# Kernel optimization log

Hardware: AMD Instinct MI355X
Metric: run time of the kernel (lower is better)

Reference implementation:

```python
import jax, jax.numpy as jnp
import numpy as np

N_QUBITS = 12
N_LAYERS = 3


def _apply_ry(state, theta, q):
    # state: (2,)*n real statevector; RY on qubit q
    c = jnp.cos(theta * 0.5)
    s = jnp.sin(theta * 0.5)
    st = jnp.moveaxis(state, q, 0)
    st = jnp.stack([c * st[0] - s * st[1], s * st[0] + c * st[1]])
    return jnp.moveaxis(st, 0, q)


def _apply_cz(state, q, r):
    st = jnp.moveaxis(state, (q, r), (0, 1))
    st = st.at[1, 1].multiply(-1.0)
    return jnp.moveaxis(st, (0, 1), (q, r))


def _embed(x, params):
    # angle-embedding ansatz: L layers of RY(theta[l,q]+x[q]) + CZ ring
    n = N_QUBITS
    state = jnp.zeros((2,) * n, dtype=x.dtype).at[(0,) * n].set(1.0)
    for l in range(N_LAYERS):
        for q in range(n):
            state = _apply_ry(state, params[l, q] + x[q], q)
        for q in range(n):
            state = _apply_cz(state, q, (q + 1) % n)
    return state.reshape(-1)  # (2^n,)


def setup_inputs() -> dict:
    key = jax.random.key(0)
    k1, k2, k3 = jax.random.split(key, 3)
    data = jax.random.uniform(k1, (2048, N_QUBITS), dtype=jnp.float32)
    labels = jax.random.randint(k2, (2048,), 0, 2, dtype=jnp.int32)
    params = jax.random.normal(k3, (N_LAYERS, N_QUBITS), dtype=jnp.float32)
    return {"data": data, "labels": labels, "params": params}


def reference(data, labels, params):
    # Psi[i] = U(x_i, params)|0>, k_ij = |<psi_j|psi_i>|^2 (== prob of amp 0 of U^dag(x_j)U(x_i)|0>)
    psi = jax.vmap(_embed, in_axes=(0, None))(data, params)  # (N, 2^n)
    K = jnp.square(psi @ psi.T)                              # (N, N) pairwise kernel
    lab = 2.0 * labels.astype(psi.dtype) - 1.0               # {0,1} -> {-1,+1}
    LL = jnp.outer(lab, lab)
    kernel_polarity = jnp.sum(LL * K)
    square_sum_k = jnp.sum(K * K)
    square_sum_l = jnp.sum(LL * LL)
    return kernel_polarity / jnp.sqrt(square_sum_k * square_sum_l)
```

## Files before the change

kernel.cpp:

```cpp
#include <hip/hip_runtime.h>
#include <math.h>

#define NQ    12
#define DIM   4096
#define K_EXT 4096
#define KSL   1024
#define NSAMP 2048
#define NLAY  3
#define NT2   16
#define NTRI2 136
#define NSLICE 4
#define BK    64

typedef __attribute__((ext_vector_type(8)))  short bf16x8;
typedef __attribute__((ext_vector_type(16))) float floatx16;

__device__ __forceinline__ unsigned short f32_to_bf16(float x) {
    unsigned u = __builtin_bit_cast(unsigned, x);
    u += 0x7FFFu + ((u >> 16) & 1u);
    return (unsigned short)(u >> 16);
}

__device__ __forceinline__ void gl_lds16(const unsigned short* g, unsigned short* l) {
    __builtin_amdgcn_global_load_lds(
        (const __attribute__((address_space(1))) unsigned int*)g,
        (__attribute__((address_space(3))) unsigned int*)l,
        16, 0, 0);
}

__device__ __forceinline__ void tri_decode(int bid, int& bi, int& bj) {
    int i = (int)((33.0 - sqrt(33.0*33.0 - 8.0*(double)bid)) * 0.5);
    int start = i*(33-i)/2;
    while (bid < start)               { --i; start = i*(33-i)/2; }
    while (bid >= start + (NT2 - i))  { start += NT2 - i; ++i; }
    bi = i; bj = i + (bid - start);
}

__global__ __launch_bounds__(256) void sim_kernel(const float* __restrict__ data,
                                                  const float* __restrict__ params,
                                                  unsigned short* __restrict__ pe)
{
    __shared__ float CS[2*36], SN[2*36];
    __shared__ float trans[2][4608];
    const int tid  = threadIdx.x;
    const int wave = tid >> 6, lane = tid & 63;
    const int sidx = wave >> 1;
    const int w    = wave & 1;
    const int smp  = blockIdx.x * 2 + sidx;

    if (w == 0 && lane < NLAY*NQ) {
        const int q = lane % NQ;
        const float th = 0.5f * (params[lane] + data[smp*NQ + q]);
        CS[sidx*36 + lane] = cosf(th);
        SN[sidx*36 + lane] = sinf(th);
    }
    __syncthreads();

    float v[32];

    float* buf = trans[sidx];
    float* wb  = buf + 36*lane + 2304*w;
    const float* rb = buf + ((lane>>2)&15) + 16*w + 36*(lane&3);

    {
        const float* cs = &CS[sidx*36];
        const float* sn = &SN[sidx*36];
        const int hi = (lane >> 2) & 15;
        float fx = ((lane & 1) ? sn[0] : cs[0]) * ((lane & 2) ? sn[1] : cs[1]);
        fx *= ((hi & 1) ? sn[7]  : cs[7]);
        fx *= ((hi & 2) ? sn[8]  : cs[8]);
        fx *= ((hi & 4) ? sn[9]  : cs[9]);
        fx *= ((hi & 8) ? sn[10] : cs[10]);
        fx *= (w ? sn[11] : cs[11]);
        v[0] = fx * cs[2];
        v[1] = fx * sn[2];
        #pragma unroll
        for (int b = 1; b < 5; ++b) {
            const int M = 1 << b;
            #pragma unroll
            for (int r = 0; r < 32; ++r) {
                if (r < M) {
                    v[r | M] = v[r] * sn[2 + b];
                    v[r]     = v[r] * cs[2 + b];
                }
            }
        }
        const int Base = (lane & 3) | (hi << 7) | (w << 11);
        #pragma unroll
        for (int r = 0; r < 32; ++r) {
            const int i  = Base | (r << 2);
            const int t  = ((i >> 1) | (i << 11)) & 0xFFF;
            const int p  = __popc(i & t) & 1;
            v[r] = __builtin_bit_cast(float, __builtin_bit_cast(int, v[r]) ^ (p << 31));
        }
    }

    #pragma unroll 1
    for (int l = 1; l < NLAY; ++l) {
        const float* cs = &CS[sidx*36 + l*NQ];
        const float* sn = &SN[sidx*36 + l*NQ];
        const int even = !(l & 1);

        {
            const int qb = even ? 7 : 2;
            #pragma unroll
            for (int b = 0; b < 5; ++b) {
                const float c = cs[qb + b], s = sn[qb + b];
                const int M = 1 << b;
                #pragma unroll
                for (int r = 0; r < 32; ++r) {
                    if (!(r & M)) {
                        const float a0 = v[r], a1 = v[r | M];
                        v[r]     = c * a0 - s * a1;
                        v[r | M] = s * a0 + c * a1;
                    }
                }
            }
        }
        {
            const float c0 = cs[0], s0 = sn[0];
            const float t0 = (lane & 1) ? s0 : -s0;
            #pragma unroll
            for (int r = 0; r < 32; ++r) {
                const int iv = __builtin_bit_cast(int, v[r]);
                const int pv = __builtin_amdgcn_update_dpp(0, iv, 0xB1, 0xF, 0xF, true);
                v[r] = c0 * v[r] + t0 * __builtin_bit_cast(float, pv);
            }
            const float c1 = cs[1], s1 = sn[1];
            const float t1 = (lane & 2) ? s1 : -s1;
            #pragma unroll
            for (int r = 0; r < 32; ++r) {
                const int iv = __builtin_bit_cast(int, v[r]);
                const int pv = __builtin_amdgcn_update_dpp(0, iv, 0x4E, 0xF, 0xF, true);
                v[r] = c1 * v[r] + t1 * __builtin_bit_cast(float, pv);
            }
        }
        __syncthreads();
        #pragma unroll
        for (int t = 0; t < 8; ++t) {
            float4 q4;
            q4.x = v[4*t]; q4.y = v[4*t+1]; q4.z = v[4*t+2]; q4.w = v[4*t+3];
            *(float4*)&wb[4*t] = q4;
        }
        __syncthreads();
        #pragma unroll
        for (int r = 0; r < 32; ++r)
            v[r] = rb[144*(r & 15) + 2304*(r >> 4)];

        {
            const int qb = even ? 2 : 7;
            #pragma unroll
            for (int b = 0; b < 5; ++b) {
                const float c = cs[qb + b], s = sn[qb + b];
                const int M = 1 << b;
                #pragma unroll
                for (int r = 0; r < 32; ++r) {
                    if (!(r & M)) {
                        const float a0 = v[r], a1 = v[r | M];
                        v[r]     = c * a0 - s * a1;
                        v[r | M] = s * a0 + c * a1;
                    }
                }
            }
        }
        {
            const int Base = even ? ((lane & 3) | (((lane >> 2) & 15) << 7) | (w << 11))
                                  : (lane | (w << 6));
            const int shift = even ? 2 : 7;
            #pragma unroll
            for (int r = 0; r < 32; ++r) {
                const int i  = Base | (r << shift);
                const int t  = ((i >> 1) | (i << 11)) & 0xFFF;
                const int p  = __popc(i & t) & 1;
                v[r] = __builtin_bit_cast(float, __builtin_bit_cast(int, v[r]) ^ (p << 31));
            }
        }
    }

    const int sw = smp & 7;
    const int ell = w*64 + lane;
    unsigned short* outb = pe + (size_t)smp * K_EXT;
    #pragma unroll
    for (int c = 0; c < 4; ++c) {
        uint4 H;
        H.x = (unsigned)f32_to_bf16(v[c*8+0]) | ((unsigned)f32_to_bf16(v[c*8+1]) << 16);
        H.y = (unsigned)f32_to_bf16(v[c*8+2]) | ((unsigned)f32_to_bf16(v[c*8+3]) << 16);
        H.z = (unsigned)f32_to_bf16(v[c*8+4]) | ((unsigned)f32_to_bf16(v[c*8+5]) << 16);
        H.w = (unsigned)f32_to_bf16(v[c*8+6]) | ((unsigned)f32_to_bf16(v[c*8+7]) << 16);
        const int gc  = 4*ell + c;
        const int pos = (gc & ~7) | ((gc ^ sw) & 7);
        *(uint4*)&outb[pos*8] = H;
    }
}

__global__ __launch_bounds__(256) void gram_partial(const unsigned short* __restrict__ pe,
                                                    float* __restrict__ Gp)
{
    __shared__ __align__(16) unsigned short stage[2][2*128*64];

    const int tid   = threadIdx.x;
    const int tile  = blockIdx.x >> 2;
    const int slice = blockIdx.x & 3;
    int bi, bj; tri_decode(tile, bi, bj);
    const int k0 = slice * KSL;

    const int wave = tid >> 6, lane = tid & 63;
    const int qr = (wave >> 1) * 64;
    const int qc = (wave &  1) * 64;
    const int mrow = lane & 31;
    const int chsel = lane >> 5;
    const int sw = mrow & 7;

    floatx16 c00, c01, c10, c11;
    #pragma unroll
    for (int i = 0; i < 16; ++i) { c00[i]=0.f; c01[i]=0.f; c10[i]=0.f; c11[i]=0.f; }

    const int mat  = wave >> 1;
    const int half = wave & 1;
    const unsigned short* gbase = pe
        + ((size_t)((mat ? bj : bi)*128 + half*64 + (lane >> 3))) * K_EXT
        + k0 + (lane & 7)*8;
    const int lofs = mat*128*64 + half*64*64;

    {
        unsigned short* l = &stage[0][lofs];
        #pragma unroll
        for (int i = 0; i < 8; ++i)
            gl_lds16(gbase + (size_t)i*8*K_EXT, l + i*512);
    }
    __syncthreads();

    int cur = 0;
    #pragma unroll 1
    for (int kk = 0; kk < KSL; kk += BK) {
        if (kk + BK < KSL) {
            unsigned short* l = &stage[cur ^ 1][lofs];
            const unsigned short* g = gbase + kk + BK;
            #pragma unroll
            for (int i = 0; i < 8; ++i)
                gl_lds16(g + (size_t)i*8*K_EXT, l + i*512);
        }

        const unsigned short* As = &stage[cur][0];
        const unsigned short* Bs = &stage[cur][128*64];
        #pragma unroll
        for (int ks = 0; ks < 4; ++ks) {
            const int ch = (ks*2 + chsel) ^ sw;
            const bf16x8 a0 = *(const bf16x8*)&As[(qr +      mrow)*64 + ch*8];
            const bf16x8 a1 = *(const bf16x8*)&As[(qr + 32 + mrow)*64 + ch*8];
            const bf16x8 b0 = *(const bf16x8*)&Bs[(qc +      mrow)*64 + ch*8];
            const bf16x8 b1 = *(const bf16x8*)&Bs[(qc + 32 + mrow)*64 + ch*8];
            c00 = __builtin_amdgcn_mfma_f32_32x32x16_bf16(a0, b0, c00, 0, 0, 0);
            c01 = __builtin_amdgcn_mfma_f32_32x32x16_bf16(a0, b1, c01, 0, 0, 0);
            c10 = __builtin_amdgcn_mfma_f32_32x32x16_bf16(a1, b0, c10, 0, 0, 0);
            c11 = __builtin_amdgcn_mfma_f32_32x32x16_bf16(a1, b1, c11, 0, 0, 0);
        }
        __syncthreads();
        cur ^= 1;
    }

    float* Gt = Gp + ((size_t)slice * NTRI2 + tile) * 16384;
    const int crow = chsel * 4;
    const int ccol = lane & 31;
    #pragma unroll
    for (int rr = 0; rr < 16; ++rr) {
        const int rl = (rr & 3) + 8*(rr >> 2) + crow;
        const int r0 = qr + rl,  r1 = qr + 32 + rl;
        const int cA = qc + ccol, cB = qc + 32 + ccol;
        Gt[r0*128 + cA] = c00[rr];
        Gt[r0*128 + cB] = c01[rr];
        Gt[r1*128 + cA] = c10[rr];
        Gt[r1*128 + cB] = c11[rr];
    }
}

__global__ __launch_bounds__(256) void gram_reduce(const float* __restrict__ Gp,
                                                   const int* __restrict__ labels,
                                                   double* __restrict__ part1,
                                                   double* __restrict__ part2)
{
    __shared__ float la[128], lb[128];
    __shared__ double red[256];
    const int tid  = threadIdx.x;
    const int tile = blockIdx.x >> 2;
    const int quar = blockIdx.x & 3;
    int bi, bj; tri_decode(tile, bi, bj);

    if (tid < 128) la[tid]       = 2.0f*(float)labels[bi*128 + tid]       - 1.0f;
    else           lb[tid - 128] = 2.0f*(float)labels[bj*128 + tid - 128] - 1.0f;
    __syncthreads();

    const size_t stride = (size_t)NTRI2 * 16384;
    const float* g0 = Gp + (size_t)tile * 16384 + quar * 4096;

    double s1 = 0.0, s2 = 0.0;
    #pragma unroll 2
    for (int u = 0; u < 16; ++u) {
        const int e  = u*256 + tid;
        const int ge = quar*4096 + e;
        float g = 0.f;
        #pragma unroll
        for (int s = 0; s < NSLICE; ++s) g += g0[e + (size_t)s*stride];
        const int row = ge >> 7, col = ge & 127;
        const float w = (bi < bj) ? 2.0f : ((row < col) ? 2.0f : ((row == col) ? 1.0f : 0.0f));
        const float g2 = g * g;
        s1 += (double)(w * la[row] * lb[col] * g2);
        const double d = (double)g2;
        s2 += (double)w * d * d;
    }

    red[tid] = s1; __syncthreads();
    for (int off = 128; off; off >>= 1) { if (tid < off) red[tid] += red[tid+off]; __syncthreads(); }
    if (tid == 0) part1[blockIdx.x] = red[0];
    __syncthreads();
    red[tid] = s2; __syncthreads();
    for (int off = 128; off; off >>= 1) { if (tid < off) red[tid] += red[tid+off]; __syncthreads(); }
    if (tid == 0) part2[blockIdx.x] = red[0];
}

__global__ __launch_bounds__(256) void finalize_kernel(const double* __restrict__ part1,
                                                       const double* __restrict__ part2,
                                                       float* __restrict__ out)
{
    __shared__ double r1[256], r2[256];
    const int tid = threadIdx.x;
    double a = 0.0, b = 0.0;
    #pragma unroll
    for (int u = 0; u < 3; ++u) {
        const int s = tid + u*256;
        if (s < NTRI2*4) { a += part1[s]; b += part2[s]; }
    }
    r1[tid] = a; r2[tid] = b; __syncthreads();
    for (int off = 128; off; off >>= 1) {
        if (tid < off) { r1[tid] += r1[tid+off]; r2[tid] += r2[tid+off]; }
        __syncthreads();
    }
    if (tid == 0) out[0] = (float)(r1[0] / (sqrt(r2[0]) * (double)NSAMP));
}

extern "C" void kernel_launch(void* const* d_in, const int* in_sizes, int n_in,
                              void* d_out, int out_size, void* d_ws, size_t ws_size,
                              hipStream_t stream)
{
    const float* data   = (const float*)d_in[0];
    const int*   labels = (const int*)d_in[1];
    const float* params = (const float*)d_in[2];

    double* part1 = (double*)d_ws;
    double* part2 = part1 + 768;
    unsigned short* psi = (unsigned short*)((char*)d_ws + 16384);
    float* Gp = (float*)((char*)d_ws + 16384 + (size_t)NSAMP*K_EXT*2);

    sim_kernel<<<NSAMP/2, 256, 0, stream>>>(data, params, psi);
    gram_partial<<<NTRI2*NSLICE, 256, 0, stream>>>(psi, Gp);
    gram_reduce<<<NTRI2*4, 256, 0, stream>>>(Gp, labels, part1, part2);
    finalize_kernel<<<1, 256, 0, stream>>>(part1, part2, (float*)d_out);
}
```

Measured before the change: 124.0 us.

## Single-buffer LDS with register prefetch in gram_partial for higher occupancy

Replaces the double-buffered direct global-to-LDS staging with a single LDS buffer. The next K-chunk is prefetched into registers while MFMAs run on the current chunk, then written to LDS between two barriers. Halving shared memory and adding launch_bounds(256,2) aims to fit more blocks per CU so more latency is hidden. The cost is an extra barrier per iteration, more VGPR pressure, and plain register stores to LDS instead of the async LDS-load path.

Result: slower. 196.2 us (+58.3%).

```diff
diff --git a/kernel.cpp b/kernel.cpp
--- a/kernel.cpp
+++ b/kernel.cpp
@@ -193,10 +193,10 @@
     }
 }
 
-__global__ __launch_bounds__(256) void gram_partial(const unsigned short* __restrict__ pe,
-                                                    float* __restrict__ Gp)
-{
-    __shared__ __align__(16) unsigned short stage[2][2*128*64];
+__global__ __launch_bounds__(256, 2) void gram_partial(const unsigned short* __restrict__ pe,
+                                                       float* __restrict__ Gp)
+{
+    __shared__ __align__(16) unsigned short stage[2*128*64];
 
     const int tid   = threadIdx.x;
     const int tile  = blockIdx.x >> 2;
@@ -222,27 +222,24 @@
         + k0 + (lane & 7)*8;
     const int lofs = mat*128*64 + half*64*64;
 
-    {
-        unsigned short* l = &stage[0][lofs];
-        #pragma unroll
-        for (int i = 0; i < 8; ++i)
-            gl_lds16(gbase + (size_t)i*8*K_EXT, l + i*512);
-    }
+    const unsigned short* As = stage;
+    const unsigned short* Bs = stage + 128*64;
+
+    #pragma unroll
+    for (int i = 0; i < 8; ++i)
+        gl_lds16(gbase + (size_t)i*8*K_EXT, stage + lofs + i*512);
     __syncthreads();
 
-    int cur = 0;
     #pragma unroll 1
-    for (int kk = 0; kk < KSL; kk += BK) {
-        if (kk + BK < KSL) {
-            unsigned short* l = &stage[cur ^ 1][lofs];
+    for (int kk = 0; kk < KSL - BK; kk += BK) {
+        uint4 p[8];
+        {
             const unsigned short* g = gbase + kk + BK;
             #pragma unroll
             for (int i = 0; i < 8; ++i)
-                gl_lds16(g + (size_t)i*8*K_EXT, l + i*512);
-        }
-
-        const unsigned short* As = &stage[cur][0];
-        const unsigned short* Bs = &stage[cur][128*64];
+                p[i] = *(const uint4*)(g + (size_t)i*8*K_EXT);
+        }
+
         #pragma unroll
         for (int ks = 0; ks < 4; ++ks) {
             const int ch = (ks*2 + chsel) ^ sw;
@@ -255,8 +252,25 @@
             c10 = __builtin_amdgcn_mfma_f32_32x32x16_bf16(a1, b0, c10, 0, 0, 0);
             c11 = __builtin_amdgcn_mfma_f32_32x32x16_bf16(a1, b1, c11, 0, 0, 0);
         }
-        __syncthreads();
-        cur ^= 1;
+
+        __syncthreads();
+        #pragma unroll
+        for (int i = 0; i < 8; ++i)
+            *(uint4*)&stage[lofs + i*512 + lane*8] = p[i];
+        __syncthreads();
+    }
+
+    #pragma unroll
+    for (int ks = 0; ks < 4; ++ks) {
+        const int ch = (ks*2 + chsel) ^ sw;
+        const bf16x8 a0 = *(const bf16x8*)&As[(qr +      mrow)*64 + ch*8];
+        const bf16x8 a1 = *(const bf16x8*)&As[(qr + 32 + mrow)*64 + ch*8];
+        const bf16x8 b0 = *(const bf16x8*)&Bs[(qc +      mrow)*64 + ch*8];
+        const bf16x8 b1 = *(const bf16x8*)&Bs[(qc + 32 + mrow)*64 + ch*8];
+        c00 = __builtin_amdgcn_mfma_f32_32x32x16_bf16(a0, b0, c00, 0, 0, 0);
+        c01 = __builtin_amdgcn_mfma_f32_32x32x16_bf16(a0, b1, c01, 0, 0, 0);
+        c10 = __builtin_amdgcn_mfma_f32_32x32x16_bf16(a1, b0, c10, 0, 0, 0);
+        c11 = __builtin_amdgcn_mfma_f32_32x32x16_bf16(a1, b1, c11, 0, 0, 0);
     }
 
     float* Gt = Gp + ((size_t)slice * NTRI2 + tile) * 16384;
```
